# Performance work log

Hardware: AMD Instinct MI355X
Metric: run time of the kernel (lower is better)

## Reference

```python
import jax, jax.numpy as jnp
import numpy as np
from jax import lax

STATE_SIZE = 16

def _sobel_kernels(state_size):
    sx = jnp.array([[-1., 0., 1.], [-2., 0., 2.], [-1., 0., 1.]], dtype=jnp.float32)
    sy = sx.T
    # depthwise OIHW with feature_group_count=C: [C, 1, 3, 3]
    kx = jnp.tile(sx[None, None], (state_size, 1, 1, 1))
    ky = jnp.tile(sy[None, None], (state_size, 1, 1, 1))
    return kx, ky

def setup_inputs() -> dict:
    key = jax.random.key(0)
    k1, k2, k3 = jax.random.split(key, 3)
    B, C, H, W = 32, STATE_SIZE, 256, 256
    x = jax.random.normal(k1, (B, C, H, W), dtype=jnp.float32)
    w1 = jax.random.normal(k2, (128, 3 * C, 1, 1), dtype=jnp.float32) * 0.05
    w2 = jax.random.normal(k3, (C, 128, 1, 1), dtype=jnp.float32) * 0.05
    return {"x": x, "w1": w1, "w2": w2}

def reference(x, w1, w2):
    C = x.shape[1]
    kx, ky = _sobel_kernels(C)
    dn = ("NCHW", "OIHW", "NCHW")
    grad_x = lax.conv_general_dilated(x, kx, (1, 1), "SAME",
                                      dimension_numbers=dn, feature_group_count=C)
    grad_y = lax.conv_general_dilated(x, ky, (1, 1), "SAME",
                                      dimension_numbers=dn, feature_group_count=C)
    cat = jnp.concatenate([x, grad_x, grad_y], axis=1)  # [B, 3C, H, W]
    # 1x1 convs == per-pixel matmuls
    h = jnp.einsum("bchw,oc->bohw", cat, w1[:, :, 0, 0])  # [B,128,H,W]
    h = jax.nn.relu(h)
    update = jnp.einsum("bchw,oc->bohw", h, w2[:, :, 0, 0])  # [B,C,H,W]
    return update
```

## Files before the change

kernel.cpp:

```cpp
#include <hip/hip_runtime.h>

#define CIN 16
#define HH 256
#define WW 256
#define HID 128
#define KEFF 144
#define WS_W_BYTES (HID * KEFF * 2 + CIN * HID * 2)
#define X2_OFF_SHORTS 20480

typedef short short8b __attribute__((ext_vector_type(8)));
typedef float f32x4 __attribute__((ext_vector_type(4)));

__device__ __forceinline__ unsigned short f2bf(float f) {
    union { float f; unsigned int u; } v; v.f = f;
    unsigned int u = v.u;
    return (unsigned short)((u + 0x7fffu + ((u >> 16) & 1u)) >> 16);
}

__global__ __launch_bounds__(256) void build_weff(
    const float* __restrict__ w1, const float* __restrict__ w2,
    unsigned short* __restrict__ ws)
{
    const float SX[9] = {-1.f, 0.f, 1.f, -2.f, 0.f, 2.f, -1.f, 0.f, 1.f};
    const float SY[9] = {-1.f, -2.f, -1.f, 0.f, 0.f, 0.f, 1.f, 2.f, 1.f};
    const int idx = blockIdx.x * 256 + threadIdx.x;
    if (idx < HID * KEFF) {
        const int o = idx / KEFF, r = idx % KEFF;
        const int tap = r >> 4, c = r & 15;
        float v = w1[o * 48 + 16 + c] * SX[tap] + w1[o * 48 + 32 + c] * SY[tap];
        if (tap == 4) v += w1[o * 48 + c];
        ws[idx] = f2bf(v);
    } else if (idx < HID * KEFF + CIN * HID) {
        ws[idx] = f2bf(w2[idx - HID * KEFF]);
    }
}

__global__ __launch_bounds__(256) void nchw_to_nhwc(
    const float* __restrict__ x, unsigned short* __restrict__ x2)
{
    const int bi = blockIdx.x;
    const int b = bi >> 8, ii = bi & 255;
    const int jj = threadIdx.x;
    short8b lo, hi;
    #pragma unroll
    for (int c = 0; c < 8; ++c) {
        lo[c] = (short)f2bf(x[((size_t)(b * CIN + c) * HH + ii) * WW + jj]);
        hi[c] = (short)f2bf(x[((size_t)(b * CIN + c + 8) * HH + ii) * WW + jj]);
    }
    unsigned short* dst = x2 + ((size_t)(b * HH + ii) * WW + jj) * 16;
    *(short8b*)dst       = lo;
    *(short8b*)(dst + 8) = hi;
}

#define SM6_XL  0
#define SM6_HB  19584
#define SM6_ZR  35968
#define SM6_TOT 36000

__global__ __launch_bounds__(256, 2) void updatenet_v14(
    const unsigned short* __restrict__ ws,
    float* __restrict__ out)
{
    __shared__ __align__(16) unsigned char smem[SM6_TOT];
    unsigned short* xl   = (unsigned short*)(smem + SM6_XL);
    unsigned short* zreg = (unsigned short*)(smem + SM6_ZR);

    const int b  = blockIdx.z;
    const int i0 = blockIdx.y * 32;
    const int j0 = blockIdx.x * 16;
    const int t  = threadIdx.x;

    {
        const unsigned short* x2 = ws + X2_OFF_SHORTS;
        for (int idx = t; idx < 34 * 18 * 2; idx += 256) {
            const int ri = idx / 36, rem = idx % 36;
            const int rj = rem >> 1, half = rem & 1;
            const int ii = i0 + ri - 1, jj = j0 + rj - 1;
            short8b v = (short8b)0;
            if (ii >= 0 && ii < HH && jj >= 0 && jj < WW)
                v = *(const short8b*)(x2 + ((size_t)(b * HH + ii) * WW + jj) * 16 + half * 8);
            *(short8b*)(xl + (ri * 18 + rj) * 16 + half * 8) = v;
        }
        if (t < 2) *(short8b*)(zreg + t * 8) = (short8b)0;
    }

    const int wv   = t >> 6;
    const int lane = t & 63;
    const int p    = wv >> 1;
    const int q    = wv & 1;
    const int g    = lane >> 4;
    const int nn   = lane & 15;
    const int gh   = g >> 1, gl = g & 1;

    short8b aW1[4][5];
    #pragma unroll
    for (int mt = 0; mt < 4; ++mt)
        #pragma unroll
        for (int ks = 0; ks < 5; ++ks) {
            const int ak = (ks == 4) ? (128 + 8 * gl) : (32 * ks + 8 * g);
            aW1[mt][ks] = *(const short8b*)(ws + (size_t)(64 * q + 16 * mt + nn) * KEFF + ak);
        }
    short8b aW2[4];
    #pragma unroll
    for (int ks = 0; ks < 4; ++ks)
        aW2[ks] = *(const short8b*)(ws + HID * KEFF + nn * HID + 32 * ks + 8 * g);

    int off[5];
    #pragma unroll
    for (int ks = 0; ks < 5; ++ks) {
        int tap = 2 * ks + gh;
        if (tap > 8) tap = 8;
        off[ks] = ((tap / 3) * 18 + (tap % 3)) * 32 + gl * 16;
    }

    unsigned char* hb_pair = smem + SM6_HB + p * 8192;
    const int xmask = (nn & 7) << 4;

    __syncthreads();

    for (int s = 0; s < 16; ++s) {
        const int row = 16 * p + s;
        const unsigned char* xbase = (const unsigned char*)xl + (row * 18 + nn) * 32;

        f32x4 acc[4];
        #pragma unroll
        for (int mt = 0; mt < 4; ++mt) acc[mt] = (f32x4)0.f;

        #pragma unroll
        for (int ks = 0; ks < 5; ++ks) {
            const unsigned char* bp = (ks == 4 && gh) ? (const unsigned char*)(zreg + gl * 8)
                                                      : xbase + off[ks];
            const short8b bfrag = *(const short8b*)bp;
            #pragma unroll
            for (int mt = 0; mt < 4; ++mt)
                acc[mt] = __builtin_amdgcn_mfma_f32_16x16x32_bf16(aW1[mt][ks], bfrag, acc[mt], 0, 0, 0);
        }

        unsigned char* hph = hb_pair + (s & 1) * 4096;
        #pragma unroll
        for (int mt = 0; mt < 4; ++mt) {
            const unsigned int lo = (unsigned int)f2bf(fmaxf(acc[mt][0], 0.f))
                                  | ((unsigned int)f2bf(fmaxf(acc[mt][1], 0.f)) << 16);
            const unsigned int hi = (unsigned int)f2bf(fmaxf(acc[mt][2], 0.f))
                                  | ((unsigned int)f2bf(fmaxf(acc[mt][3], 0.f)) << 16);
            uint2 u; u.x = lo; u.y = hi;
            const int wb = (nn << 8) + ((64 * q + 16 * mt + 4 * g) << 1);
            *(uint2*)(hph + (wb ^ xmask)) = u;
        }

        __syncthreads();

        if (q == (s & 1)) {
            f32x4 a2 = (f32x4)0.f;
            #pragma unroll
            for (int ks2 = 0; ks2 < 4; ++ks2) {
                const int rb = (nn << 8) + ((32 * ks2 + 8 * g) << 1);
                const short8b bh = *(const short8b*)(hph + (rb ^ xmask));
                a2 = __builtin_amdgcn_mfma_f32_16x16x32_bf16(aW2[ks2], bh, a2, 0, 0, 0);
            }
            const int oi = i0 + row, oj = j0 + nn;
            float* op = out + ((size_t)(b * CIN + 4 * g) * HH + oi) * WW + oj;
            #pragma unroll
            for (int r = 0; r < 4; ++r)
                op[(size_t)r * HH * WW] = a2[r];
        }
    }
}

__global__ __launch_bounds__(256, 2) void updatenet_v8m(
    const float* __restrict__ x,
    const unsigned short* __restrict__ ws,
    float* __restrict__ out)
{
    __shared__ __align__(16) unsigned char smem[SM6_TOT];
    unsigned short* xl   = (unsigned short*)(smem + SM6_XL);
    unsigned short* zreg = (unsigned short*)(smem + SM6_ZR);

    const int b  = blockIdx.z;
    const int i0 = blockIdx.y * 32;
    const int j0 = blockIdx.x * 16;
    const int t  = threadIdx.x;

    {
        const size_t cs = (size_t)HH * WW;
        for (int pidx = t; pidx < 34 * 18; pidx += 256) {
            const int ri = pidx / 18, rj = pidx % 18;
            const int ii = i0 + ri - 1, jj = j0 + rj - 1;
            const bool ok = (ii >= 0) & (ii < HH) & (jj >= 0) & (jj < WW);
            const float* xp = x + ((size_t)b * CIN * HH + ii) * WW + jj;
            short8b s0, s1;
            #pragma unroll
            for (int c = 0; c < 8; ++c) {
                s0[c] = ok ? (short)f2bf(xp[c * cs]) : (short)0;
                s1[c] = ok ? (short)f2bf(xp[(c + 8) * cs]) : (short)0;
            }
            *(short8b*)(xl + pidx * 16)     = s0;
            *(short8b*)(xl + pidx * 16 + 8) = s1;
        }
        if (t < 2) *(short8b*)(zreg + t * 8) = (short8b)0;
    }

    const int wv   = t >> 6;
    const int lane = t & 63;
    const int p    = wv >> 1;
    const int q    = wv & 1;
    const int g    = lane >> 4;
    const int nn   = lane & 15;
    const int gh   = g >> 1, gl = g & 1;

    short8b aW1[4][5];
    #pragma unroll
    for (int mt = 0; mt < 4; ++mt)
        #pragma unroll
        for (int ks = 0; ks < 5; ++ks) {
            const int ak = (ks == 4) ? (128 + 8 * gl) : (32 * ks + 8 * g);
            aW1[mt][ks] = *(const short8b*)(ws + (size_t)(64 * q + 16 * mt + nn) * KEFF + ak);
        }
    short8b aW2[4];
    #pragma unroll
    for (int ks = 0; ks < 4; ++ks)
        aW2[ks] = *(const short8b*)(ws + HID * KEFF + nn * HID + 32 * ks + 8 * g);

    int off[5];
    #pragma unroll
    for (int ks = 0; ks < 5; ++ks) {
        int tap = 2 * ks + gh;
        if (tap > 8) tap = 8;
        off[ks] = ((tap / 3) * 18 + (tap % 3)) * 32 + gl * 16;
    }

    unsigned char* hb_pair = smem + SM6_HB + p * 8192;
    const int xmask = (nn & 7) << 4;

    __syncthreads();

    for (int s = 0; s < 16; ++s) {
        const int row = 16 * p + s;
        const unsigned char* xbase = (const unsigned char*)xl + (row * 18 + nn) * 32;

        f32x4 acc[4];
        #pragma unroll
        for (int mt = 0; mt < 4; ++mt) acc[mt] = (f32x4)0.f;

        #pragma unroll
        for (int ks = 0; ks < 5; ++ks) {
            const unsigned char* bp = (ks == 4 && gh) ? (const unsigned char*)(zreg + gl * 8)
                                                      : xbase + off[ks];
            const short8b bfrag = *(const short8b*)bp;
            #pragma unroll
            for (int mt = 0; mt < 4; ++mt)
                acc[mt] = __builtin_amdgcn_mfma_f32_16x16x32_bf16(aW1[mt][ks], bfrag, acc[mt], 0, 0, 0);
        }

        unsigned char* hph = hb_pair + (s & 1) * 4096;
        #pragma unroll
        for (int mt = 0; mt < 4; ++mt) {
            const unsigned int lo = (unsigned int)f2bf(fmaxf(acc[mt][0], 0.f))
                                  | ((unsigned int)f2bf(fmaxf(acc[mt][1], 0.f)) << 16);
            const unsigned int hi = (unsigned int)f2bf(fmaxf(acc[mt][2], 0.f))
                                  | ((unsigned int)f2bf(fmaxf(acc[mt][3], 0.f)) << 16);
            uint2 u; u.x = lo; u.y = hi;
            const int wb = (nn << 8) + ((64 * q + 16 * mt + 4 * g) << 1);
            *(uint2*)(hph + (wb ^ xmask)) = u;
        }

        __syncthreads();

        if (q == (s & 1)) {
            f32x4 a2 = (f32x4)0.f;
            #pragma unroll
            for (int ks2 = 0; ks2 < 4; ++ks2) {
                const int rb = (nn << 8) + ((32 * ks2 + 8 * g) << 1);
                const short8b bh = *(const short8b*)(hph + (rb ^ xmask));
                a2 = __builtin_amdgcn_mfma_f32_16x16x32_bf16(aW2[ks2], bh, a2, 0, 0, 0);
            }
            const int oi = i0 + row, oj = j0 + nn;
            float* op = out + ((size_t)(b * CIN + 4 * g) * HH + oi) * WW + oj;
            #pragma unroll
            for (int r = 0; r < 4; ++r)
                op[(size_t)r * HH * WW] = a2[r];
        }
    }
}

#define SM_WEFF  0
#define SM_GUARD 36864
#define SM_W2B   36880
#define SM_XL    41232
#define SM_ZREG  60816
#define SM_HALL  60848
#define SM_TOTAL 78256

__global__ __launch_bounds__(256, 2) void updatenet_fallback(
    const float* __restrict__ x, const float* __restrict__ w1f,
    const float* __restrict__ w2f, float* __restrict__ out)
{
    __shared__ __align__(16) unsigned char smem[SM_TOTAL];
    unsigned short* weff = (unsigned short*)(smem + SM_WEFF);
    unsigned short* w2b  = (unsigned short*)(smem + SM_W2B);
    unsigned short* xl   = (unsigned short*)(smem + SM_XL);
    unsigned short* zreg = (unsigned short*)(smem + SM_ZREG);

    const int b  = blockIdx.z;
    const int i0 = blockIdx.y * 32;
    const int j0 = blockIdx.x * 16;
    const int t  = threadIdx.x;

    for (int idx = t; idx < HID * KEFF; idx += 256) {
        const float SX[9] = {-1.f, 0.f, 1.f, -2.f, 0.f, 2.f, -1.f, 0.f, 1.f};
        const float SY[9] = {-1.f, -2.f, -1.f, 0.f, 0.f, 0.f, 1.f, 2.f, 1.f};
        const int o = idx / KEFF, r = idx % KEFF;
        const int tap = r >> 4, cc = r & 15;
        float v = w1f[o * 48 + 16 + cc] * SX[tap] + w1f[o * 48 + 32 + cc] * SY[tap];
        if (tap == 4) v += w1f[o * 48 + cc];
        weff[idx] = f2bf(v);
    }
    for (int idx = t; idx < CIN * HID; idx += 256)
        w2b[(idx >> 7) * 136 + (idx & 127)] = f2bf(w2f[idx]);

    {
        const size_t cs = (size_t)HH * WW;
        for (int pp = t; pp < 34 * 18; pp += 256) {
            const int ri = pp / 18, rj = pp % 18;
            const int ii = i0 + ri - 1, jj = j0 + rj - 1;
            const bool ok = (ii >= 0) & (ii < HH) & (jj >= 0) & (jj < WW);
            const float* xp = x + ((size_t)b * CIN * HH + ii) * WW + jj;
            short8b s0, s1;
            #pragma unroll
            for (int c = 0; c < 8; ++c) {
                s0[c] = ok ? (short)f2bf(xp[c * cs]) : (short)0;
                s1[c] = ok ? (short)f2bf(xp[(c + 8) * cs]) : (short)0;
            }
            *(short8b*)(xl + pp * 16)     = s0;
            *(short8b*)(xl + pp * 16 + 8) = s1;
        }
        if (t < 2) *(short8b*)(zreg + t * 8) = (short8b)0;
        if (t == 2) *(short8b*)(smem + SM_GUARD) = (short8b)0;
    }
    __syncthreads();

    const int w = t >> 6, lane = t & 63;
    const int g = lane >> 4, nn = lane & 15;
    const int gh = g >> 1, gl = g & 1;

    short8b aW1[8][5];
    #pragma unroll
    for (int m = 0; m < 8; ++m)
        #pragma unroll
        for (int ks = 0; ks < 5; ++ks) {
            const int ak = (ks == 4) ? (128 + 8 * gl) : (32 * ks + 8 * g);
            aW1[m][ks] = *(const short8b*)(weff + (16 * m + nn) * KEFF + ak);
        }

    int off[5];
    #pragma unroll
    for (int ks = 0; ks < 5; ++ks) {
        int tap = 2 * ks + gh;
        if (tap > 8) tap = 8;
        off[ks] = ((tap / 3) * 18 + (tap % 3)) * 32 + gl * 16;
    }

    unsigned short* hb = (unsigned short*)(smem + SM_HALL) + w * (16 * 136);

    for (int nt = 0; nt < 8; ++nt) {
        const int i = 8 * w + nt;
        const unsigned char* xbase = (const unsigned char*)xl + (i * 18 + nn) * 32;
        f32x4 acc[8];
        #pragma unroll
        for (int m = 0; m < 8; ++m) acc[m] = (f32x4)0.f;
        #pragma unroll
        for (int ks = 0; ks < 5; ++ks) {
            const unsigned char* bp = (ks == 4 && gh) ? (const unsigned char*)(zreg + gl * 8)
                                                      : xbase + off[ks];
            const short8b bfrag = *(const short8b*)bp;
            #pragma unroll
            for (int m = 0; m < 8; ++m)
                acc[m] = __builtin_amdgcn_mfma_f32_16x16x32_bf16(aW1[m][ks], bfrag, acc[m], 0, 0, 0);
        }
        #pragma unroll
        for (int m = 0; m < 8; ++m) {
            const unsigned int lo = (unsigned int)f2bf(fmaxf(acc[m][0], 0.f))
                                  | ((unsigned int)f2bf(fmaxf(acc[m][1], 0.f)) << 16);
            const unsigned int hi = (unsigned int)f2bf(fmaxf(acc[m][2], 0.f))
                                  | ((unsigned int)f2bf(fmaxf(acc[m][3], 0.f)) << 16);
            uint2 u; u.x = lo; u.y = hi;
            *(uint2*)(hb + nn * 136 + 16 * m + 4 * g) = u;
        }
        asm volatile("s_waitcnt lgkmcnt(0)" ::: "memory");
        f32x4 a2 = (f32x4)0.f;
        #pragma unroll
        for (int ks = 0; ks < 4; ++ks) {
            const short8b aw2 = *(const short8b*)(w2b + nn * 136 + 32 * ks + 8 * g);
            const short8b bh  = *(const short8b*)(hb + nn * 136 + 32 * ks + 8 * g);
            a2 = __builtin_amdgcn_mfma_f32_16x16x32_bf16(aw2, bh, a2, 0, 0, 0);
        }
        const int oi = i0 + i, oj = j0 + nn;
        float* op = out + ((size_t)(b * CIN + 4 * g) * HH + oi) * WW + oj;
        #pragma unroll
        for (int r = 0; r < 4; ++r)
            op[(size_t)r * HH * WW] = a2[r];
    }
}

extern "C" void kernel_launch(void* const* d_in, const int* in_sizes, int n_in,
                              void* d_out, int out_size, void* d_ws, size_t ws_size,
                              hipStream_t stream) {
    const float* x  = (const float*)d_in[0];
    const float* w1 = (const float*)d_in[1];
    const float* w2 = (const float*)d_in[2];
    float* out = (float*)d_out;

    const int Bn = in_sizes[0] / (CIN * HH * WW);
    dim3 grid(WW / 16, HH / 32, Bn);

    const size_t x2_bytes = (size_t)Bn * CIN * HH * WW * 2;

    if (ws_size >= (size_t)WS_W_BYTES + x2_bytes) {
        unsigned short* ws = (unsigned short*)d_ws;
        build_weff<<<(HID * KEFF + CIN * HID + 255) / 256, 256, 0, stream>>>(w1, w2, ws);
        nchw_to_nhwc<<<Bn * HH, 256, 0, stream>>>(x, ws + X2_OFF_SHORTS);
        updatenet_v14<<<grid, 256, 0, stream>>>(ws, out);
    } else if (ws_size >= (size_t)WS_W_BYTES) {
        unsigned short* ws = (unsigned short*)d_ws;
        build_weff<<<(HID * KEFF + CIN * HID + 255) / 256, 256, 0, stream>>>(w1, w2, ws);
        updatenet_v8m<<<grid, 256, 0, stream>>>(x, ws, out);
    } else {
        updatenet_fallback<<<grid, 256, 0, stream>>>(x, w1, w2, out);
    }
}
```

Measured before the change: 139.9 us.

## Process two rows per phase in fused updatenet kernel and use packed bf16 convert

The main loop now handles two output rows per iteration. It issues 8 independent MFMA chains for the first layer instead of 4 and halves the number of block-wide barriers. The hidden-activation LDS buffer doubles to hold two rows per ping-pong slot, bringing shared memory to about 52KB per block. ReLU outputs are converted with the hardware v_cvt_pk_bf16_f32 instruction instead of the manual rounding code. The trade-off is higher LDS use and more accumulator registers, which may reduce occupancy, and inline asm volatile may limit scheduling.

New measurement: 126.5 us (median of 3 runs). 9.6% less time.

```diff
diff --git a/kernel.cpp b/kernel.cpp
--- a/kernel.cpp
+++ b/kernel.cpp
@@ -15,6 +15,12 @@
     union { float f; unsigned int u; } v; v.f = f;
     unsigned int u = v.u;
     return (unsigned short)((u + 0x7fffu + ((u >> 16) & 1u)) >> 16);
+}
+
+__device__ __forceinline__ unsigned int cvtpk_bf16(float a, float b) {
+    unsigned int r;
+    asm volatile("v_cvt_pk_bf16_f32 %0, %1, %2" : "=v"(r) : "v"(a), "v"(b));
+    return r;
 }
 
 __global__ __launch_bounds__(256) void build_weff(
@@ -52,18 +58,18 @@
     *(short8b*)(dst + 8) = hi;
 }
 
-#define SM6_XL  0
-#define SM6_HB  19584
-#define SM6_ZR  35968
-#define SM6_TOT 36000
-
-__global__ __launch_bounds__(256, 2) void updatenet_v14(
+#define SME_XL  0
+#define SME_HB  19584
+#define SME_ZR  52352
+#define SME_TOT 52384
+
+__global__ __launch_bounds__(256, 2) void updatenet_v15(
     const unsigned short* __restrict__ ws,
     float* __restrict__ out)
 {
-    __shared__ __align__(16) unsigned char smem[SM6_TOT];
-    unsigned short* xl   = (unsigned short*)(smem + SM6_XL);
-    unsigned short* zreg = (unsigned short*)(smem + SM6_ZR);
+    __shared__ __align__(16) unsigned char smem[SME_TOT];
+    unsigned short* xl   = (unsigned short*)(smem + SME_XL);
+    unsigned short* zreg = (unsigned short*)(smem + SME_ZR);
 
     const int b  = blockIdx.z;
     const int i0 = blockIdx.y * 32;
@@ -113,59 +119,79 @@
         off[ks] = ((tap / 3) * 18 + (tap % 3)) * 32 + gl * 16;
     }
 
-    unsigned char* hb_pair = smem + SM6_HB + p * 8192;
+    unsigned char* hb_p = smem + SME_HB + p * 16384;
     const int xmask = (nn & 7) << 4;
 
     __syncthreads();
 
-    for (int s = 0; s < 16; ++s) {
-        const int row = 16 * p + s;
-        const unsigned char* xbase = (const unsigned char*)xl + (row * 18 + nn) * 32;
-
-        f32x4 acc[4];
-        #pragma unroll
-        for (int mt = 0; mt < 4; ++mt) acc[mt] = (f32x4)0.f;
-
-        #pragma unroll
-        for (int ks = 0; ks < 5; ++ks) {
-            const unsigned char* bp = (ks == 4 && gh) ? (const unsigned char*)(zreg + gl * 8)
-                                                      : xbase + off[ks];
-            const short8b bfrag = *(const short8b*)bp;
-            #pragma unroll
-            for (int mt = 0; mt < 4; ++mt)
-                acc[mt] = __builtin_amdgcn_mfma_f32_16x16x32_bf16(aW1[mt][ks], bfrag, acc[mt], 0, 0, 0);
-        }
-
-        unsigned char* hph = hb_pair + (s & 1) * 4096;
+    for (int phs = 0; phs < 8; ++phs) {
+        const int r0 = 16 * p + 2 * phs;
+
+        f32x4 acc[4][2];
         #pragma unroll
         for (int mt = 0; mt < 4; ++mt) {
-            const unsigned int lo = (unsigned int)f2bf(fmaxf(acc[mt][0], 0.f))
-                                  | ((unsigned int)f2bf(fmaxf(acc[mt][1], 0.f)) << 16);
-            const unsigned int hi = (unsigned int)f2bf(fmaxf(acc[mt][2], 0.f))
-                                  | ((unsigned int)f2bf(fmaxf(acc[mt][3], 0.f)) << 16);
-            uint2 u; u.x = lo; u.y = hi;
-            const int wb = (nn << 8) + ((64 * q + 16 * mt + 4 * g) << 1);
-            *(uint2*)(hph + (wb ^ xmask)) = u;
+            acc[mt][0] = (f32x4)0.f;
+            acc[mt][1] = (f32x4)0.f;
+        }
+
+        #pragma unroll
+        for (int ks = 0; ks < 5; ++ks) {
+            short8b Bf[2];
+            #pragma unroll
+            for (int rr = 0; rr < 2; ++rr) {
+                const unsigned char* bp = (ks == 4 && gh)
+                    ? (const unsigned char*)(zreg + gl * 8)
+                    : (const unsigned char*)xl + ((r0 + rr) * 18 + nn) * 32 + off[ks];
+                Bf[rr] = *(const short8b*)bp;
+            }
+            #pragma unroll
+            for (int mt = 0; mt < 4; ++mt) {
+                acc[mt][0] = __builtin_amdgcn_mfma_f32_16x16x32_bf16(aW1[mt][ks], Bf[0], acc[mt][0], 0, 0, 0);
+                acc[mt][1] = __builtin_amdgcn_mfma_f32_16x16x32_bf16(aW1[mt][ks], Bf[1], acc[mt][1], 0, 0, 0);
+            }
+        }
+
+        unsigned char* hpb = hb_p + (phs & 1) * 8192;
+        #pragma unroll
+        for (int rr = 0; rr < 2; ++rr) {
+            unsigned char* slab = hpb + rr * 4096;
+            #pragma unroll
+            for (int mt = 0; mt < 4; ++mt) {
+                uint2 u;
+                u.x = cvtpk_bf16(fmaxf(acc[mt][rr][0], 0.f), fmaxf(acc[mt][rr][1], 0.f));
+                u.y = cvtpk_bf16(fmaxf(acc[mt][rr][2], 0.f), fmaxf(acc[mt][rr][3], 0.f));
+                const int wb = (nn << 8) + ((64 * q + 16 * mt + 4 * g) << 1);
+                *(uint2*)(slab + (wb ^ xmask)) = u;
+            }
         }
 
         __syncthreads();
 
-        if (q == (s & 1)) {
-            f32x4 a2 = (f32x4)0.f;
-            #pragma unroll
-            for (int ks2 = 0; ks2 < 4; ++ks2) {
-                const int rb = (nn << 8) + ((32 * ks2 + 8 * g) << 1);
-                const short8b bh = *(const short8b*)(hph + (rb ^ xmask));
-                a2 = __builtin_amdgcn_mfma_f32_16x16x32_bf16(aW2[ks2], bh, a2, 0, 0, 0);
-            }
-            const int oi = i0 + row, oj = j0 + nn;
-            float* op = out + ((size_t)(b * CIN + 4 * g) * HH + oi) * WW + oj;
-            #pragma unroll
-            for (int r = 0; r < 4; ++r)
-                op[(size_t)r * HH * WW] = a2[r];
-        }
-    }
-}
+        if (q == (phs & 1)) {
+            #pragma unroll
+            for (int rr = 0; rr < 2; ++rr) {
+                const unsigned char* slab = hpb + rr * 4096;
+                f32x4 a2 = (f32x4)0.f;
+                #pragma unroll
+                for (int ks2 = 0; ks2 < 4; ++ks2) {
+                    const int rb = (nn << 8) + ((32 * ks2 + 8 * g) << 1);
+                    const short8b bh = *(const short8b*)(slab + (rb ^ xmask));
+                    a2 = __builtin_amdgcn_mfma_f32_16x16x32_bf16(aW2[ks2], bh, a2, 0, 0, 0);
+                }
+                const int oi = i0 + r0 + rr, oj = j0 + nn;
+                float* op = out + ((size_t)(b * CIN + 4 * g) * HH + oi) * WW + oj;
+                #pragma unroll
+                for (int r = 0; r < 4; ++r)
+                    op[(size_t)r * HH * WW] = a2[r];
+            }
+        }
+    }
+}
+
+#define SM6_XL  0
+#define SM6_HB  19584
+#define SM6_ZR  35968
+#define SM6_TOT 36000
 
 __global__ __launch_bounds__(256, 2) void updatenet_v8m(
     const float* __restrict__ x,
@@ -419,7 +445,7 @@
         unsigned short* ws = (unsigned short*)d_ws;
         build_weff<<<(HID * KEFF + CIN * HID + 255) / 256, 256, 0, stream>>>(w1, w2, ws);
         nchw_to_nhwc<<<Bn * HH, 256, 0, stream>>>(x, ws + X2_OFF_SHORTS);
-        updatenet_v14<<<grid, 256, 0, stream>>>(ws, out);
+        updatenet_v15<<<grid, 256, 0, stream>>>(ws, out);
     } else if (ws_size >= (size_t)WS_W_BYTES) {
         unsigned short* ws = (unsigned short*)d_ws;
         build_weff<<<(HID * KEFF + CIN * HID + 255) / 256, 256, 0, stream>>>(w1, w2, ws);
```
